# Performance work log

Measured on AMD Instinct MI355X. Metric: run time of the kernel, lower is better.

Reference implementation:

```python
import jax
import jax.numpy as jnp
from jax import lax
import numpy as np

INPUT_DIM = 784
HIDDEN_DIM = 1024
BATCH = 256
N_BINS = 10


def setup_inputs() -> dict:
    key = jax.random.key(0)
    k1, k2, k3, k4, k5 = jax.random.split(key, 5)
    # kaiming-normal-ish init scales (faithful in spirit; exact values irrelevant for math)
    W = jax.random.normal(k1, (HIDDEN_DIM, INPUT_DIM), dtype=jnp.float32) * np.sqrt(2.0 / INPUT_DIM)
    c = jnp.zeros((HIDDEN_DIM, 1), dtype=jnp.float32)
    V = jax.random.normal(k2, (INPUT_DIM, HIDDEN_DIM, N_BINS), dtype=jnp.float32) * np.sqrt(2.0 / N_BINS)
    b = jnp.zeros((INPUT_DIM, N_BINS), dtype=jnp.float32)
    x = jax.random.randint(k3, (BATCH, INPUT_DIM), 0, N_BINS, dtype=jnp.int32)
    return {"x": x, "W": W, "c": c, "V": V, "b": b}


def reference(x, W, c, V, b):
    # x: [B, D] int pixel bins; W: [H, D]; c: [H, 1]; V: [D, H, 10]; b: [D, 10]
    B = x.shape[0]
    xf = x.astype(jnp.float32)  # [B, D]
    a0 = jnp.broadcast_to(c[:, 0][None, :], (B, W.shape[0]))  # [B, H]

    def step(a, inp):
        Vi, bi, Wi, xi = inp  # Vi:[H,10], bi:[10], Wi:[H], xi:[B]
        h = jax.nn.sigmoid(a)                       # [B, H]
        p = jax.nn.softmax(h @ Vi + bi, axis=1)     # [B, 10]
        a = a + xi[:, None] * Wi[None, :]           # rank-1 update, matches x_i @ W[:,i].T
        return a, p

    _, p_seq = lax.scan(step, a0, (V, b, W.T, xf.T))  # p_seq: [D, B, 10]
    p_hat = jnp.transpose(p_seq, (1, 2, 0))            # [B, 10, D] == torch.stack(p_hat, dim=2)
    return p_hat
```

## Files before the change

### kernel.cpp

```cpp
#include <hip/hip_runtime.h>
#include <stdint.h>

#define D_DIM 784
#define H_DIM 1024
#define B_DIM 256
#define NBIN  10
#define G_CH  8
#define T_CH  98
#define BT    16
#define BF    2
#define LOG2E 1.4426950408889634f

typedef _Float16 half8_t  __attribute__((ext_vector_type(8)));
typedef __fp16   fp16x2_t __attribute__((ext_vector_type(2)));
typedef float    float4_t __attribute__((ext_vector_type(4)));

__global__ void k_transpose(const float* __restrict__ W, float* __restrict__ Wt2) {
    __shared__ float t[64][65];
    int j0 = blockIdx.x * 64, h0 = blockIdx.y * 64;
    int tj = threadIdx.x & 63, tr = threadIdx.x >> 6;
    int j = j0 + tj;
    #pragma unroll
    for (int r = 0; r < 16; ++r) {
        int hh = tr * 16 + r;
        t[hh][tj] = (j < D_DIM) ? W[(size_t)(h0 + hh) * D_DIM + j] : 0.0f;
    }
    __syncthreads();
    #pragma unroll
    for (int r = 0; r < 16; ++r) {
        int jj = tr * 16 + r;
        int jo = j0 + jj;
        if (jo < D_DIM) Wt2[(size_t)jo * H_DIM + h0 + tj] = t[tj][jj] * LOG2E;
    }
}

__global__ void k_vbprep(const float* __restrict__ V, _Float16* __restrict__ VB) {
    int i   = blockIdx.x;
    int tid = threadIdx.x;
    __shared__ __align__(16) float vsf[H_DIM * NBIN];
    const float4* src = (const float4*)(V + (size_t)i * H_DIM * NBIN);
    #pragma unroll
    for (int q = 0; q < 10; ++q) {
        float4 v = src[q * 256 + tid];
        *((float4*)&vsf[(q * 256 + tid) * 4]) = v;
    }
    __syncthreads();
    #pragma unroll
    for (int q = 0; q < 8; ++q) {
        int pair = q * 256 + tid;
        int kk = pair >> 6, l = pair & 63;
        int n = l & 15, hb = kk * 32 + ((l >> 4) & 3) * 8;
        union { _Float16 h[8]; uint4 u; } o;
        #pragma unroll
        for (int jj = 0; jj < 8; ++jj)
            o.h[jj] = (_Float16)((n < NBIN) ? vsf[(hb + jj) * NBIN + n] : 0.0f);
        ((uint4*)VB)[(size_t)i * 2048 + pair] = o.u;
    }
}

template<typename CT>
__global__ void k_pscan(const float* __restrict__ Wt2, const int* __restrict__ x,
                        const float* __restrict__ c, CT* __restrict__ PA) {
    int b0 = blockIdx.x * BF;
    int h  = blockIdx.y * 256 + threadIdx.x;
    __shared__ float xs[BF][D_DIM];
    for (int q = threadIdx.x; q < BF * (D_DIM / 4); q += 256) {
        int bb = q / (D_DIM / 4), r = q % (D_DIM / 4);
        int4 xi = ((const int4*)(x + (size_t)(b0 + bb) * D_DIM))[r];
        float4 xf = make_float4((float)xi.x, (float)xi.y, (float)xi.z, (float)xi.w);
        *((float4*)&xs[bb][r * 4]) = xf;
    }
    float acc0 = c[h] * LOG2E, acc1 = acc0;
    __syncthreads();
    for (int t = 0; t < T_CH; ++t) {
        PA[((size_t)t * B_DIM + b0 + 0) * H_DIM + h] = (CT)acc0;
        PA[((size_t)t * B_DIM + b0 + 1) * H_DIM + h] = (CT)acc1;
        #pragma unroll
        for (int j = 0; j < G_CH; ++j) {
            float wv = Wt2[(size_t)(t * G_CH + j) * H_DIM + h];
            acc0 += xs[0][t * G_CH + j] * wv;
            acc1 += xs[1][t * G_CH + j] * wv;
        }
    }
}

template<typename CT>
__global__ __launch_bounds__(256, 3)
void k_main(const float* __restrict__ Wt2, const _Float16* __restrict__ VB,
            const CT* __restrict__ PA, const int* __restrict__ x,
            const float* __restrict__ bias, float* __restrict__ out) {
    int bt  = blockIdx.x;
    int tc  = blockIdx.y;
    int tid = threadIdx.x;
    int w   = tid >> 6;
    int l   = tid & 63;
    int bl  = l & 15;
    int kg  = l >> 4;
    int bg  = bt * BT + bl;
    int i0  = tc * G_CH;

    __shared__ float red[4][64][5];
    __shared__ float bs[G_CH][16];
    __shared__ __align__(16) float plds[BT][NBIN][12];

    {
        int ii = tid >> 4, n = tid & 15;
        if (ii < G_CH) bs[ii][n] = (n < NBIN) ? bias[(size_t)(i0 + ii) * NBIN + n] : 0.0f;
    }

    float a[8][8];
    {
        const CT* src = PA + ((size_t)tc * B_DIM + bg) * H_DIM + w * 256 + kg * 8;
        #pragma unroll
        for (int m = 0; m < 8; ++m)
            #pragma unroll
            for (int j = 0; j < 8; ++j)
                a[m][j] = (float)src[m * 32 + j];
    }
    __syncthreads();

    const float4* wt4 = (const float4*)Wt2;
    const uint4* vbbase = (const uint4*)VB;
    #pragma unroll 1
    for (int ii = 0; ii < G_CH; ++ii) {
        int i = i0 + ii;
        float xvf = (float)x[(size_t)bg * D_DIM + i];

        uint4 vb[8];
        const uint4* vbp = vbbase + ((size_t)i * 32 + w * 8) * 64 + l;
        #pragma unroll
        for (int m = 0; m < 8; ++m) vb[m] = vbp[m * 64];

        float4_t cfrag = {0.f, 0.f, 0.f, 0.f};
        #pragma unroll
        for (int m = 0; m < 8; ++m) {
            union { half8_t h8; uint u32[4]; } af;
            #pragma unroll
            for (int p = 0; p < 4; ++p) {
                float s0 = __builtin_amdgcn_rcpf(1.0f + __builtin_amdgcn_exp2f(-a[m][2 * p]));
                float s1 = __builtin_amdgcn_rcpf(1.0f + __builtin_amdgcn_exp2f(-a[m][2 * p + 1]));
                union { fp16x2_t v; uint u; } cv;
                cv.v = __builtin_amdgcn_cvt_pkrtz(s0, s1);
                af.u32[p] = cv.u;
            }
            union { half8_t h8; uint4 u; } bf;
            bf.u = vb[m];
            cfrag = __builtin_amdgcn_mfma_f32_16x16x32_f16(af.h8, bf.h8, cfrag, 0, 0, 0);

            int hb = (w * 256 + kg * 8 + m * 32) >> 2;
            float4 w0 = wt4[(size_t)i * (H_DIM / 4) + hb];
            float4 w1 = wt4[(size_t)i * (H_DIM / 4) + hb + 1];
            a[m][0] += xvf * w0.x; a[m][1] += xvf * w0.y; a[m][2] += xvf * w0.z; a[m][3] += xvf * w0.w;
            a[m][4] += xvf * w1.x; a[m][5] += xvf * w1.y; a[m][6] += xvf * w1.z; a[m][7] += xvf * w1.w;
        }

        red[w][l][0] = cfrag[0]; red[w][l][1] = cfrag[1];
        red[w][l][2] = cfrag[2]; red[w][l][3] = cfrag[3];
        __syncthreads();
        float tot = red[0][l][w] + red[1][l][w] + red[2][l][w] + red[3][l][w];
        int n = bl;
        float v = (n < NBIN) ? tot + bs[ii][n] : -3.0e38f;
        float vm = v;
        vm = fmaxf(vm, __shfl_xor(vm, 1));
        vm = fmaxf(vm, __shfl_xor(vm, 2));
        vm = fmaxf(vm, __shfl_xor(vm, 4));
        vm = fmaxf(vm, __shfl_xor(vm, 8));
        float e = __builtin_amdgcn_exp2f((v - vm) * LOG2E);
        float ss = e;
        ss += __shfl_xor(ss, 1); ss += __shfl_xor(ss, 2);
        ss += __shfl_xor(ss, 4); ss += __shfl_xor(ss, 8);
        float p = e * __builtin_amdgcn_rcpf(ss);
        if (n < NBIN) plds[kg * 4 + w][n][ii] = p;
        __syncthreads();
    }

    if (tid < BT * NBIN) {
        int bb = tid / NBIN, n = tid % NBIN;
        size_t base = ((size_t)(bt * BT + bb) * NBIN + n) * D_DIM + i0;
        #pragma unroll
        for (int q = 0; q < 2; ++q) {
            float4 v = *((float4*)&plds[bb][n][q * 4]);
            *((float4*)(out + base + q * 4)) = v;
        }
    }
}

extern "C" void kernel_launch(void* const* d_in, const int* in_sizes, int n_in,
                              void* d_out, int out_size, void* d_ws, size_t ws_size,
                              hipStream_t stream) {
    const int*   x    = (const int*)d_in[0];
    const float* W    = (const float*)d_in[1];
    const float* c    = (const float*)d_in[2];
    const float* V    = (const float*)d_in[3];
    const float* bias = (const float*)d_in[4];
    float* out = (float*)d_out;

    char* ws = (char*)d_ws;
    size_t off = 0;
    float* Wt2 = (float*)(ws + off);
    off += (size_t)D_DIM * H_DIM * sizeof(float);
    off = (off + 255) & ~(size_t)255;
    _Float16* VB = (_Float16*)(ws + off);
    off += (size_t)D_DIM * 32 * 64 * 8 * sizeof(_Float16);
    off = (off + 255) & ~(size_t)255;
    size_t pa_f32 = (size_t)T_CH * B_DIM * H_DIM * sizeof(float);
    bool f32ck = (off + pa_f32) <= ws_size;

    k_transpose<<<dim3(13, 16), 256, 0, stream>>>(W, Wt2);
    k_vbprep<<<dim3(D_DIM), 256, 0, stream>>>(V, VB);

    if (f32ck) {
        float* PA = (float*)(ws + off);
        k_pscan<float><<<dim3(B_DIM / BF, 4), 256, 0, stream>>>(Wt2, x, c, PA);
        k_main<float><<<dim3(B_DIM / BT, T_CH), 256, 0, stream>>>(Wt2, VB, PA, x, bias, out);
    } else {
        _Float16* PA = (_Float16*)(ws + off);
        k_pscan<_Float16><<<dim3(B_DIM / BF, 4), 256, 0, stream>>>(Wt2, x, c, PA);
        k_main<_Float16><<<dim3(B_DIM / BT, T_CH), 256, 0, stream>>>(Wt2, VB, PA, x, bias, out);
    }
}
```

Baseline: 210.4 us.

## Double-buffer softmax reduction, stage W rows in LDS, widen prefix-scan batch

In the main kernel, the softmax for step ii-1 now runs after step ii's V loads are issued, using a double-buffered reduction array. This removes one __syncthreads per step and overlaps the reduction with the MFMA work. The 8 W rows for the chunk are staged in shared memory, and the x values are loaded up front instead of once per step. The prefix-scan kernel processes 4 batch rows per thread instead of 2, and the main kernel's launch bound drops from 3 to 2 blocks per CU. That lowers occupancy, and the added LDS use could limit residency further.

After: 210.6 us. About the same (+0.1%).

```diff
diff --git a/kernel.cpp b/kernel.cpp
--- a/kernel.cpp
+++ b/kernel.cpp
@@ -8,7 +8,7 @@
 #define G_CH  8
 #define T_CH  98
 #define BT    16
-#define BF    2
+#define BF    4
 #define LOG2E 1.4426950408889634f
 
 typedef _Float16 half8_t  __attribute__((ext_vector_type(8)));
@@ -70,22 +70,27 @@
         float4 xf = make_float4((float)xi.x, (float)xi.y, (float)xi.z, (float)xi.w);
         *((float4*)&xs[bb][r * 4]) = xf;
     }
-    float acc0 = c[h] * LOG2E, acc1 = acc0;
+    float acc[BF];
+    float cv = c[h] * LOG2E;
+    #pragma unroll
+    for (int bb = 0; bb < BF; ++bb) acc[bb] = cv;
     __syncthreads();
     for (int t = 0; t < T_CH; ++t) {
-        PA[((size_t)t * B_DIM + b0 + 0) * H_DIM + h] = (CT)acc0;
-        PA[((size_t)t * B_DIM + b0 + 1) * H_DIM + h] = (CT)acc1;
+        #pragma unroll
+        for (int bb = 0; bb < BF; ++bb)
+            PA[((size_t)t * B_DIM + b0 + bb) * H_DIM + h] = (CT)acc[bb];
         #pragma unroll
         for (int j = 0; j < G_CH; ++j) {
             float wv = Wt2[(size_t)(t * G_CH + j) * H_DIM + h];
-            acc0 += xs[0][t * G_CH + j] * wv;
-            acc1 += xs[1][t * G_CH + j] * wv;
+            #pragma unroll
+            for (int bb = 0; bb < BF; ++bb)
+                acc[bb] += xs[bb][t * G_CH + j] * wv;
         }
     }
 }
 
 template<typename CT>
-__global__ __launch_bounds__(256, 3)
+__global__ __launch_bounds__(256, 2)
 void k_main(const float* __restrict__ Wt2, const _Float16* __restrict__ VB,
             const CT* __restrict__ PA, const int* __restrict__ x,
             const float* __restrict__ bias, float* __restrict__ out) {
@@ -99,7 +104,8 @@
     int bg  = bt * BT + bl;
     int i0  = tc * G_CH;
 
-    __shared__ float red[4][64][5];
+    __shared__ __align__(16) float wlds[G_CH][H_DIM];
+    __shared__ float red[2][4][64][5];
     __shared__ float bs[G_CH][16];
     __shared__ __align__(16) float plds[BT][NBIN][12];
 
@@ -107,7 +113,20 @@
         int ii = tid >> 4, n = tid & 15;
         if (ii < G_CH) bs[ii][n] = (n < NBIN) ? bias[(size_t)(i0 + ii) * NBIN + n] : 0.0f;
     }
-
+    {
+        #pragma unroll
+        for (int r = 0; r < G_CH; ++r) {
+            float4 v = ((const float4*)(Wt2 + (size_t)(i0 + r) * H_DIM))[tid];
+            *((float4*)&wlds[r][tid * 4]) = v;
+        }
+    }
+    float xvf[G_CH];
+    {
+        const int4* xp = (const int4*)(x + (size_t)bg * D_DIM + i0);
+        int4 x0 = xp[0], x1 = xp[1];
+        xvf[0] = (float)x0.x; xvf[1] = (float)x0.y; xvf[2] = (float)x0.z; xvf[3] = (float)x0.w;
+        xvf[4] = (float)x1.x; xvf[5] = (float)x1.y; xvf[6] = (float)x1.z; xvf[7] = (float)x1.w;
+    }
     float a[8][8];
     {
         const CT* src = PA + ((size_t)tc * B_DIM + bg) * H_DIM + w * 256 + kg * 8;
@@ -119,18 +138,36 @@
     }
     __syncthreads();
 
-    const float4* wt4 = (const float4*)Wt2;
     const uint4* vbbase = (const uint4*)VB;
     #pragma unroll 1
     for (int ii = 0; ii < G_CH; ++ii) {
         int i = i0 + ii;
-        float xvf = (float)x[(size_t)bg * D_DIM + i];
+        int par = ii & 1;
 
         uint4 vb[8];
         const uint4* vbp = vbbase + ((size_t)i * 32 + w * 8) * 64 + l;
         #pragma unroll
         for (int m = 0; m < 8; ++m) vb[m] = vbp[m * 64];
 
+        if (ii > 0) {
+            int ip = ii - 1, pp = par ^ 1;
+            float tot = red[pp][0][l][w] + red[pp][1][l][w] + red[pp][2][l][w] + red[pp][3][l][w];
+            int n = bl;
+            float v = (n < NBIN) ? tot + bs[ip][n] : -3.0e38f;
+            float vm = v;
+            vm = fmaxf(vm, __shfl_xor(vm, 1));
+            vm = fmaxf(vm, __shfl_xor(vm, 2));
+            vm = fmaxf(vm, __shfl_xor(vm, 4));
+            vm = fmaxf(vm, __shfl_xor(vm, 8));
+            float e = __builtin_amdgcn_exp2f((v - vm) * LOG2E);
+            float ss = e;
+            ss += __shfl_xor(ss, 1); ss += __shfl_xor(ss, 2);
+            ss += __shfl_xor(ss, 4); ss += __shfl_xor(ss, 8);
+            float p = e * __builtin_amdgcn_rcpf(ss);
+            if (n < NBIN) plds[kg * 4 + w][n][ip] = p;
+        }
+
+        float xf = xvf[ii];
         float4_t cfrag = {0.f, 0.f, 0.f, 0.f};
         #pragma unroll
         for (int m = 0; m < 8; ++m) {
@@ -147,19 +184,22 @@
             bf.u = vb[m];
             cfrag = __builtin_amdgcn_mfma_f32_16x16x32_f16(af.h8, bf.h8, cfrag, 0, 0, 0);
 
-            int hb = (w * 256 + kg * 8 + m * 32) >> 2;
-            float4 w0 = wt4[(size_t)i * (H_DIM / 4) + hb];
-            float4 w1 = wt4[(size_t)i * (H_DIM / 4) + hb + 1];
-            a[m][0] += xvf * w0.x; a[m][1] += xvf * w0.y; a[m][2] += xvf * w0.z; a[m][3] += xvf * w0.w;
-            a[m][4] += xvf * w1.x; a[m][5] += xvf * w1.y; a[m][6] += xvf * w1.z; a[m][7] += xvf * w1.w;
-        }
-
-        red[w][l][0] = cfrag[0]; red[w][l][1] = cfrag[1];
-        red[w][l][2] = cfrag[2]; red[w][l][3] = cfrag[3];
+            const float4* wrow = (const float4*)&wlds[ii][w * 256 + kg * 8];
+            float4 w0 = wrow[m * 8];
+            float4 w1 = wrow[m * 8 + 1];
+            a[m][0] += xf * w0.x; a[m][1] += xf * w0.y; a[m][2] += xf * w0.z; a[m][3] += xf * w0.w;
+            a[m][4] += xf * w1.x; a[m][5] += xf * w1.y; a[m][6] += xf * w1.z; a[m][7] += xf * w1.w;
+        }
+
+        red[par][w][l][0] = cfrag[0]; red[par][w][l][1] = cfrag[1];
+        red[par][w][l][2] = cfrag[2]; red[par][w][l][3] = cfrag[3];
         __syncthreads();
-        float tot = red[0][l][w] + red[1][l][w] + red[2][l][w] + red[3][l][w];
+    }
+    {
+        int ip = G_CH - 1, pp = (G_CH - 1) & 1;
+        float tot = red[pp][0][l][w] + red[pp][1][l][w] + red[pp][2][l][w] + red[pp][3][l][w];
         int n = bl;
-        float v = (n < NBIN) ? tot + bs[ii][n] : -3.0e38f;
+        float v = (n < NBIN) ? tot + bs[ip][n] : -3.0e38f;
         float vm = v;
         vm = fmaxf(vm, __shfl_xor(vm, 1));
         vm = fmaxf(vm, __shfl_xor(vm, 2));
@@ -170,9 +210,9 @@
         ss += __shfl_xor(ss, 1); ss += __shfl_xor(ss, 2);
         ss += __shfl_xor(ss, 4); ss += __shfl_xor(ss, 8);
         float p = e * __builtin_amdgcn_rcpf(ss);
-        if (n < NBIN) plds[kg * 4 + w][n][ii] = p;
-        __syncthreads();
-    }
+        if (n < NBIN) plds[kg * 4 + w][n][ip] = p;
+    }
+    __syncthreads();
 
     if (tid < BT * NBIN) {
         int bb = tid / NBIN, n = tid % NBIN;
```
